# Kernel tuning notes

Measured on AMD Instinct MI355X. Metric: run time of the kernel, lower is better.

The kernel has to match this reference:

```python
import jax, jax.numpy as jnp
import numpy as np
from jax import lax

D_MODEL = 1024
D_STATE = 16
D_CONV = 4
EXPAND = 2
D_INNER = EXPAND * D_MODEL  # 2048
DT_RANK = -(-D_MODEL // 16)  # ceil = 64
BATCH = 2
T = 1024


def setup_inputs() -> dict:
    key = jax.random.key(0)
    ks = jax.random.split(key, 9)
    s = 0.02
    x = jax.random.normal(ks[0], (BATCH, T, D_MODEL), dtype=jnp.float32)
    W_in = jax.random.normal(ks[1], (D_MODEL, 2 * D_INNER), dtype=jnp.float32) * s
    conv_w = jax.random.normal(ks[2], (D_INNER, D_CONV), dtype=jnp.float32) * 0.2
    conv_b = jax.random.normal(ks[3], (D_INNER,), dtype=jnp.float32) * 0.02
    W_xproj = jax.random.normal(ks[4], (D_INNER, DT_RANK + 2 * D_STATE), dtype=jnp.float32) * s
    W_dt = jax.random.normal(ks[5], (DT_RANK, D_INNER), dtype=jnp.float32) * s
    b_dt = jax.random.normal(ks[6], (D_INNER,), dtype=jnp.float32) * 0.02
    A_log = jnp.broadcast_to(jnp.log(jnp.arange(1, D_STATE + 1, dtype=jnp.float32)), (D_INNER, D_STATE)).copy()
    D_param = jnp.ones((D_INNER,), dtype=jnp.float32)
    W_out = jax.random.normal(ks[7], (D_INNER, D_MODEL), dtype=jnp.float32) * s
    return {"x": x, "W_in": W_in, "conv_w": conv_w, "conv_b": conv_b,
            "W_xproj": W_xproj, "W_dt": W_dt, "b_dt": b_dt,
            "A_log": A_log, "D_param": D_param, "W_out": W_out}


def _silu(u):
    return u * jax.nn.sigmoid(u)


def _forward(x, W_in, conv_w, conv_b, W_xproj, W_dt, b_dt, A_log, D_param, W_out):
    B, Tlen, _ = x.shape
    # in_proj and split into x-branch and gate z
    xz = x @ W_in                                   # (B,T,2*d_inner)
    x_b, z = jnp.split(xz, 2, axis=-1)              # each (B,T,d_inner)
    # causal depthwise conv1d: y[t] = sum_k w[:,k] * x[t-d_conv+1+k]
    xpad = jnp.pad(x_b, ((0, 0), (D_CONV - 1, 0), (0, 0)))
    xc = conv_b
    for k in range(D_CONV):
        xc = xc + xpad[:, k:k + Tlen, :] * conv_w[:, k]
    xc = _silu(xc)                                  # (B,T,d_inner)
    # SSM parameter projections
    proj = xc @ W_xproj                             # (B,T,dt_rank+2*d_state)
    delta_raw = proj[..., :DT_RANK]
    B_in = proj[..., DT_RANK:DT_RANK + D_STATE]     # (B,T,d_state)
    C_in = proj[..., DT_RANK + D_STATE:]            # (B,T,d_state)
    delta = jax.nn.softplus(delta_raw @ W_dt + b_dt)  # (B,T,d_inner)
    A = -jnp.exp(A_log)                             # (d_inner,d_state)
    A_bar = jnp.exp(delta[..., None] * A)           # (B,T,d_inner,d_state)
    Bx = delta[..., None] * B_in[:, :, None, :] * xc[..., None]  # (B,T,d_inner,d_state)

    def step(h, ins):
        a_t, bx_t, c_t, xc_t = ins
        h = a_t * h + bx_t                          # (B,d_inner,d_state)
        y_t = jnp.einsum('bds,bs->bd', h, c_t) + D_param * xc_t
        return h, y_t

    h0 = jnp.zeros((B, D_INNER, D_STATE), dtype=x.dtype)
    ins = (jnp.swapaxes(A_bar, 0, 1), jnp.swapaxes(Bx, 0, 1),
           jnp.swapaxes(C_in, 0, 1), jnp.swapaxes(xc, 0, 1))
    _, ys = lax.scan(step, h0, ins)                 # ys: (T,B,d_inner)
    y = jnp.swapaxes(ys, 0, 1) * _silu(z)           # gated
    return y @ W_out                                # (B,T,d_model)


def reference(x, W_in, conv_w, conv_b, W_xproj, W_dt, b_dt, A_log, D_param, W_out):
    return _forward(x, W_in, conv_w, conv_b, W_xproj, W_dt, b_dt, A_log, D_param, W_out)
```

## Files before the change

kernel.cpp:

```cpp
#include <hip/hip_runtime.h>
#include <math.h>

#define BATCH   2
#define TLEN    1024
#define DMODEL  1024
#define DINNER  2048
#define DSTATE  16
#define DTRANK  64
#define NPROJ   (DTRANK + 2*DSTATE)
#define CH      16
#define NCH     (TLEN / CH)

typedef __attribute__((ext_vector_type(8))) short short8;
typedef __attribute__((ext_vector_type(4))) float f32x4;

__device__ __forceinline__ float siluf(float u) {
    return u / (1.0f + __expf(-u));
}
__device__ __forceinline__ float softplusf(float x) {
    return (x > 20.0f) ? x : log1pf(__expf(x));
}
__device__ __forceinline__ unsigned short f2bf(float f) {
    union { float f; unsigned u; } v; v.f = f;
    unsigned r = v.u + 0x7FFF + ((v.u >> 16) & 1);
    return (unsigned short)(r >> 16);
}
__device__ __forceinline__ float bf2f(unsigned short u) {
    union { unsigned u; float f; } v; v.u = (unsigned)u << 16;
    return v.f;
}

#define GLOAD_LDS16(g, l) \
  __builtin_amdgcn_global_load_lds( \
     (const __attribute__((address_space(1))) unsigned int*)(g), \
     (__attribute__((address_space(3))) unsigned int*)(l), 16, 0, 0)

template<int NFRAG, int OUTBF, int EPI>
__global__ __launch_bounds__(256)
void gemm_bf16(const unsigned short* __restrict__ A, int lda,
               const unsigned short* __restrict__ BT, int ldb,
               void* __restrict__ Cv, int ldc, int kchunk,
               const float* __restrict__ bias, size_t zstride)
{
    constexpr int BN = NFRAG * 32;
    __shared__ unsigned short As[128 * 32];
    __shared__ unsigned short Bs[BN * 32];

    const int nwg = gridDim.x * gridDim.y;
    int id = blockIdx.y * gridDim.x + blockIdx.x;
    {
        const int q = nwg >> 3, r = nwg & 7, xcd = id & 7, lid = id >> 3;
        id = (xcd < r ? xcd * (q + 1) : r * (q + 1) + (xcd - r) * q) + lid;
    }
    const int bx = id % gridDim.x, by = id / gridDim.x;

    const int tid  = threadIdx.x;
    const int wid  = tid >> 6;
    const int lane = tid & 63;
    const int brow = by * 128;
    const int bcol = bx * BN;
    const int kbeg = blockIdx.z * kchunk;
    const int wr = (wid >> 1) * 64;
    const int wc = (wid & 1) * (NFRAG * 16);
    const int lrow = lane & 15;
    const int lk   = (lane >> 4) * 8;

    f32x4 acc[4][NFRAG] = {};

    for (int k0 = kbeg; k0 < kbeg + kchunk; k0 += 32) {
        #pragma unroll
        for (int it = 0; it < 2; ++it) {
            const int c = it * 256 + tid;
            const unsigned short* g = A + (size_t)(brow + (c >> 2)) * lda + k0 + (c & 3) * 8;
            GLOAD_LDS16(g, As + (size_t)(it * 256 + wid * 64) * 8);
        }
        constexpr int BCH = BN * 4;
        #pragma unroll
        for (int it = 0; it < (BCH + 255) / 256; ++it) {
            const int c = it * 256 + tid;
            if (BCH % 256 == 0 || c < BCH) {
                const unsigned short* g = BT + (size_t)(bcol + (c >> 2)) * ldb + k0 + (c & 3) * 8;
                GLOAD_LDS16(g, Bs + (size_t)(it * 256 + wid * 64) * 8);
            }
        }
        __syncthreads();

        short8 af[4], bfr[NFRAG];
        #pragma unroll
        for (int m = 0; m < 4; ++m)
            af[m] = *(const short8*)(As + (size_t)(wr + m * 16 + lrow) * 32 + lk);
        #pragma unroll
        for (int n = 0; n < NFRAG; ++n)
            bfr[n] = *(const short8*)(Bs + (size_t)(wc + n * 16 + lrow) * 32 + lk);

        #pragma unroll
        for (int m = 0; m < 4; ++m)
            #pragma unroll
            for (int n = 0; n < NFRAG; ++n)
                acc[m][n] = __builtin_amdgcn_mfma_f32_16x16x32_bf16(af[m], bfr[n], acc[m][n], 0, 0, 0);
        __syncthreads();
    }

    const size_t zoff = (size_t)blockIdx.z * zstride;
    const int crow = (lane >> 4) * 4;
    #pragma unroll
    for (int m = 0; m < 4; ++m)
        #pragma unroll
        for (int n = 0; n < NFRAG; ++n) {
            const int gc = bcol + wc + n * 16 + lrow;
            const size_t coff = zoff + (size_t)(brow + wr + m * 16 + crow) * ldc + gc;
            #pragma unroll
            for (int r = 0; r < 4; ++r) {
                float v = acc[m][n][r];
                if (EPI == 1) v = softplusf(v + bias[gc]);
                if (OUTBF)
                    ((unsigned short*)Cv)[coff + (size_t)r * ldc] = f2bf(v);
                else
                    ((float*)Cv)[coff + (size_t)r * ldc] = v;
            }
        }
}

__global__ __launch_bounds__(256)
void reduce8_dual(const float* __restrict__ in, float* __restrict__ out,
                  unsigned short* __restrict__ draw, int n, size_t zstride)
{
    const int i = blockIdx.x * 256 + threadIdx.x;
    if (i >= n) return;
    float s = 0.f;
    #pragma unroll
    for (int z = 0; z < 8; ++z) s += in[(size_t)z * zstride + i];
    out[i] = s;
    const int row = i / NPROJ;
    const int col = i - row * NPROJ;
    if (col < DTRANK) draw[(size_t)row * DTRANK + col] = f2bf(s);
}

__global__ __launch_bounds__(256)
void cast_rn(const float* __restrict__ in, unsigned short* __restrict__ out)
{
    const int i = blockIdx.x * 256 + threadIdx.x;
    float4 v = ((const float4*)in)[i];
    union { unsigned short u[4]; uint2 v2; } o;
    o.u[0] = f2bf(v.x); o.u[1] = f2bf(v.y); o.u[2] = f2bf(v.z); o.u[3] = f2bf(v.w);
    ((uint2*)out)[i] = o.v2;
}

__global__ __launch_bounds__(256)
void transpose_cast(const float* __restrict__ in, unsigned short* __restrict__ out,
                    int R, int C)
{
    __shared__ float tile[32][33];
    const int tx = threadIdx.x & 31, ty = threadIdx.x >> 5;
    const int c0 = blockIdx.x * 32, r0 = blockIdx.y * 32;
    #pragma unroll
    for (int j = 0; j < 32; j += 8)
        tile[ty + j][tx] = in[(size_t)(r0 + ty + j) * C + c0 + tx];
    __syncthreads();
    #pragma unroll
    for (int j = 0; j < 32; j += 8)
        out[(size_t)(c0 + ty + j) * R + r0 + tx] = f2bf(tile[tx][ty + j]);
}

__global__ __launch_bounds__(256)
void conv_silu(const unsigned short* __restrict__ xz, const float* __restrict__ conv_w,
               const float* __restrict__ conv_b, unsigned short* __restrict__ xc)
{
    const int idx = blockIdx.x * 256 + threadIdx.x;
    const int d = idx & (DINNER - 1);
    const int t = (idx >> 11) & (TLEN - 1);
    const int b = idx >> 21;

    const unsigned short* xb = xz + (size_t)b * TLEN * (2*DINNER) + d;
    float s = conv_b[d];
    const float4 w = *(const float4*)(conv_w + d * 4);
    const float wk[4] = {w.x, w.y, w.z, w.w};
    #pragma unroll
    for (int k = 0; k < 4; ++k) {
        const int tt = t + k - 3;
        if (tt >= 0) s = fmaf(bf2f(xb[(size_t)tt * (2*DINNER)]), wk[k], s);
    }
    xc[idx] = f2bf(siluf(s));
}

__global__ __launch_bounds__(256)
void scan1(const unsigned short* __restrict__ delta, const unsigned short* __restrict__ xc,
           const float* __restrict__ proj, const float* __restrict__ A_log,
           float* __restrict__ hloc, float* __restrict__ sumdel)
{
    const int idx = blockIdx.x * 256 + threadIdx.x;
    const int d = idx & (DINNER - 1);
    const int c = (idx >> 11) & (NCH - 1);
    const int b = idx >> 17;

    float Aa[DSTATE];
    #pragma unroll
    for (int s = 0; s < DSTATE; ++s) Aa[s] = -__expf(A_log[d * DSTATE + s]);

    float h[DSTATE];
    #pragma unroll
    for (int s = 0; s < DSTATE; ++s) h[s] = 0.f;
    float sd = 0.f;

    const int t0 = c * CH;
    const unsigned short* dptr = delta + ((size_t)(b * TLEN + t0)) * DINNER + d;
    const unsigned short* xptr = xc    + ((size_t)(b * TLEN + t0)) * DINNER + d;
    const float* pptr = proj  + ((size_t)(b * TLEN + t0)) * NPROJ;

    for (int t = 0; t < CH; ++t) {
        const float dl = bf2f(dptr[(size_t)t * DINNER]);
        const float xv = bf2f(xptr[(size_t)t * DINNER]);
        const float dx = dl * xv;
        sd += dl;
        #pragma unroll
        for (int s = 0; s < DSTATE; ++s) {
            const float ab = __expf(dl * Aa[s]);
            const float Bv = pptr[t * NPROJ + DTRANK + s];
            h[s] = fmaf(ab, h[s], dx * Bv);
        }
    }
    const size_t base = (((size_t)(b * DINNER + d)) * NCH + c) * DSTATE;
    float4* hp = (float4*)(hloc + base);
    hp[0] = make_float4(h[0],  h[1],  h[2],  h[3]);
    hp[1] = make_float4(h[4],  h[5],  h[6],  h[7]);
    hp[2] = make_float4(h[8],  h[9],  h[10], h[11]);
    hp[3] = make_float4(h[12], h[13], h[14], h[15]);
    sumdel[(size_t)(b * DINNER + d) * NCH + c] = sd;
}

__global__ __launch_bounds__(256)
void scan_combine(const float* __restrict__ hloc, const float* __restrict__ sumdel,
                  const float* __restrict__ A_log, float* __restrict__ hstart)
{
    __shared__ float hl[64 * 17];
    __shared__ float hs[64 * 17];
    const int bd   = blockIdx.x;
    const int d    = bd & (DINNER - 1);
    const int tid  = threadIdx.x;
    const int lane = tid & 63;
    const int w    = tid >> 6;

    const size_t gbase = (size_t)bd * NCH * DSTATE;
    {
        const float4 v = ((const float4*)(hloc + gbase))[tid];
        const int c = tid >> 2, s0 = (tid & 3) * 4;
        hl[c*17 + s0+0] = v.x; hl[c*17 + s0+1] = v.y;
        hl[c*17 + s0+2] = v.z; hl[c*17 + s0+3] = v.w;
    }
    const float sd = sumdel[(size_t)bd * NCH + lane];
    __syncthreads();

    #pragma unroll
    for (int q = 0; q < 4; ++q) {
        const int s = w * 4 + q;
        const float Aa = -__expf(A_log[d * DSTATE + s]);
        float A  = __expf(Aa * sd);
        float Bv = hl[lane*17 + s];
        #pragma unroll
        for (int off = 1; off < 64; off <<= 1) {
            float Ap = __shfl_up(A, off);
            float Bp = __shfl_up(Bv, off);
            if (lane >= off) { Bv = fmaf(A, Bp, Bv); A *= Ap; }
        }
        float hsv = __shfl_up(Bv, 1);
        if (lane == 0) hsv = 0.f;
        hs[lane*17 + s] = hsv;
    }
    __syncthreads();
    {
        const int c = tid >> 2, s0 = (tid & 3) * 4;
        float4 v = make_float4(hs[c*17 + s0+0], hs[c*17 + s0+1],
                               hs[c*17 + s0+2], hs[c*17 + s0+3]);
        ((float4*)(hstart + gbase))[tid] = v;
    }
}

__global__ __launch_bounds__(256)
void scan2(const unsigned short* __restrict__ delta, const unsigned short* __restrict__ xc,
           const float* __restrict__ proj, const float* __restrict__ A_log,
           const float* __restrict__ D_param, const unsigned short* __restrict__ xz,
           const float* __restrict__ hstart, unsigned short* __restrict__ y)
{
    const int idx = blockIdx.x * 256 + threadIdx.x;
    const int d = idx & (DINNER - 1);
    const int c = (idx >> 11) & (NCH - 1);
    const int b = idx >> 17;

    float Aa[DSTATE];
    #pragma unroll
    for (int s = 0; s < DSTATE; ++s) Aa[s] = -__expf(A_log[d * DSTATE + s]);

    float h[DSTATE];
    const size_t hbase = (((size_t)(b * DINNER + d)) * NCH + c) * DSTATE;
    {
        const float4* hp = (const float4*)(hstart + hbase);
        float4 v0 = hp[0], v1 = hp[1], v2 = hp[2], v3 = hp[3];
        h[0]=v0.x; h[1]=v0.y; h[2]=v0.z; h[3]=v0.w;
        h[4]=v1.x; h[5]=v1.y; h[6]=v1.z; h[7]=v1.w;
        h[8]=v2.x; h[9]=v2.y; h[10]=v2.z; h[11]=v2.w;
        h[12]=v3.x; h[13]=v3.y; h[14]=v3.z; h[15]=v3.w;
    }

    const float Dp = D_param[d];
    const int t0 = c * CH;
    const unsigned short* dptr = delta + ((size_t)(b * TLEN + t0)) * DINNER + d;
    const unsigned short* xptr = xc    + ((size_t)(b * TLEN + t0)) * DINNER + d;
    const float* pptr = proj  + ((size_t)(b * TLEN + t0)) * NPROJ;
    const unsigned short* zptr = xz + ((size_t)(b * TLEN + t0)) * (2*DINNER) + DINNER + d;
    unsigned short* yptr = y + ((size_t)(b * TLEN + t0)) * DINNER + d;

    for (int t = 0; t < CH; ++t) {
        const float dl = bf2f(dptr[(size_t)t * DINNER]);
        const float xv = bf2f(xptr[(size_t)t * DINNER]);
        const float dx = dl * xv;
        float yt = 0.f;
        #pragma unroll
        for (int s = 0; s < DSTATE; ++s) {
            const float ab = __expf(dl * Aa[s]);
            const float Bv = pptr[t * NPROJ + DTRANK + s];
            h[s] = fmaf(ab, h[s], dx * Bv);
            const float Cv = pptr[t * NPROJ + DTRANK + DSTATE + s];
            yt = fmaf(h[s], Cv, yt);
        }
        yt = fmaf(Dp, xv, yt);
        const float z = bf2f(zptr[(size_t)t * (2*DINNER)]);
        yptr[(size_t)t * DINNER] = f2bf(yt * siluf(z));
    }
}

extern "C" void kernel_launch(void* const* d_in, const int* in_sizes, int n_in,
                              void* d_out, int out_size, void* d_ws, size_t ws_size,
                              hipStream_t stream)
{
    const float* x      = (const float*)d_in[0];
    const float* W_in   = (const float*)d_in[1];
    const float* conv_w = (const float*)d_in[2];
    const float* conv_b = (const float*)d_in[3];
    const float* W_xproj= (const float*)d_in[4];
    const float* W_dt   = (const float*)d_in[5];
    const float* b_dt   = (const float*)d_in[6];
    const float* A_log  = (const float*)d_in[7];
    const float* D_param= (const float*)d_in[8];
    const float* W_out  = (const float*)d_in[9];
    float* out = (float*)d_out;

    float* ws = (float*)d_ws;
    unsigned short* xz_bf    = (unsigned short*)ws;
    unsigned short* xc_bf    = (unsigned short*)(ws + 4194304);
    float*          proj     = ws + 6291456;
    unsigned short* delta_bf = (unsigned short*)(ws + 6488064);
    float*          hloc     = ws + 8585216;
    float*          sumdel   = ws + 12779520;
    float*          hstart   = ws + 13041664;
    float*          projp    = hloc;
    unsigned short* draw_bf  = (unsigned short*)(hloc + 1572864);
    unsigned short* yb_bf    = (unsigned short*)hloc;
    unsigned short* wt_out   = (unsigned short*)(hloc + 2097152);
    unsigned short* x_bf     = (unsigned short*)hstart;
    unsigned short* wt_in    = (unsigned short*)(hstart + 1048576);
    unsigned short* wxp_t    = (unsigned short*)(hstart + 3145728);
    unsigned short* wdt_t    = (unsigned short*)(hstart + 3244032);

    dim3 blk(256);

    cast_rn<<<2048, blk, 0, stream>>>(x, x_bf);
    transpose_cast<<<dim3(2*DINNER/32, DMODEL/32), blk, 0, stream>>>(W_in, wt_in, DMODEL, 2*DINNER);
    gemm_bf16<4,1,0><<<dim3(2*DINNER/128, 2048/128), blk, 0, stream>>>(
        x_bf, DMODEL, wt_in, DMODEL, xz_bf, 2*DINNER, DMODEL, nullptr, 0);

    conv_silu<<<(BATCH*TLEN*DINNER)/256, blk, 0, stream>>>(xz_bf, conv_w, conv_b, xc_bf);

    transpose_cast<<<dim3(NPROJ/32, DINNER/32), blk, 0, stream>>>(W_xproj, wxp_t, DINNER, NPROJ);
    gemm_bf16<3,0,0><<<dim3(1, 2048/128, 8), blk, 0, stream>>>(
        xc_bf, DINNER, wxp_t, DINNER, projp, NPROJ, DINNER/8, nullptr, 196608);
    reduce8_dual<<<768, blk, 0, stream>>>(projp, proj, draw_bf, 196608, 196608);

    transpose_cast<<<dim3(DINNER/32, DTRANK/32), blk, 0, stream>>>(W_dt, wdt_t, DTRANK, DINNER);
    gemm_bf16<4,1,1><<<dim3(2048/128, 2048/128), blk, 0, stream>>>(
        draw_bf, DTRANK, wdt_t, DTRANK, delta_bf, DINNER, DTRANK, b_dt, 0);

    scan1<<<(BATCH*NCH*DINNER)/256, blk, 0, stream>>>(delta_bf, xc_bf, proj, A_log, hloc, sumdel);
    scan_combine<<<BATCH*DINNER, blk, 0, stream>>>(hloc, sumdel, A_log, hstart);
    transpose_cast<<<dim3(DMODEL/32, DINNER/32), blk, 0, stream>>>(W_out, wt_out, DINNER, DMODEL);
    scan2<<<(BATCH*NCH*DINNER)/256, blk, 0, stream>>>(delta_bf, xc_bf, proj, A_log, D_param, xz_bf, hstart, yb_bf);

    gemm_bf16<2,0,0><<<dim3(DMODEL/64, 2048/128), blk, 0, stream>>>(
        yb_bf, DINNER, wt_out, DINNER, out, DMODEL, DINNER, nullptr, 0);
}
```

Baseline: 284.6 us.

## Fuse weight prep kernels, double scan chunk size, store chunk states in bf16

Merges the input cast and four weight transpose-casts into one prep kernel, which cuts several launches. Doubles the scan chunk length so there are half as many chunks, which halves the inter-chunk state traffic and shrinks the combine scan to 32 lanes. Stores per-chunk local and start states as bf16 instead of fp32, cutting their memory traffic at some precision cost. The workspace is re-laid out so buffers no longer alias, and scan1/scan2 now launch half as many threads, each doing more sequential work.

```diff
diff --git a/kernel.cpp b/kernel.cpp
--- a/kernel.cpp
+++ b/kernel.cpp
@@ -8,7 +8,7 @@
 #define DSTATE  16
 #define DTRANK  64
 #define NPROJ   (DTRANK + 2*DSTATE)
-#define CH      16
+#define CH      32
 #define NCH     (TLEN / CH)
 
 typedef __attribute__((ext_vector_type(8))) short short8;
@@ -121,6 +121,52 @@
         }
 }
 
+__device__ __forceinline__ void tile_transpose(float (*tile)[33],
+        const float* __restrict__ in, unsigned short* __restrict__ out,
+        int R, int C, int bx, int by, int tx, int ty)
+{
+    const int c0 = bx * 32, r0 = by * 32;
+    #pragma unroll
+    for (int j = 0; j < 32; j += 8)
+        tile[ty + j][tx] = in[(size_t)(r0 + ty + j) * C + c0 + tx];
+    __syncthreads();
+    #pragma unroll
+    for (int j = 0; j < 32; j += 8)
+        out[(size_t)(c0 + ty + j) * R + r0 + tx] = f2bf(tile[tx][ty + j]);
+}
+
+__global__ __launch_bounds__(256)
+void prep(const float* __restrict__ x, const float* __restrict__ W_in,
+          const float* __restrict__ W_xproj, const float* __restrict__ W_dt,
+          const float* __restrict__ W_out,
+          unsigned short* __restrict__ x_bf, unsigned short* __restrict__ wt_in,
+          unsigned short* __restrict__ wxp_t, unsigned short* __restrict__ wdt_t,
+          unsigned short* __restrict__ wt_out)
+{
+    __shared__ float tile[32][33];
+    const int blk = blockIdx.x;
+    const int tx = threadIdx.x & 31, ty = threadIdx.x >> 5;
+    if (blk < 2048) {
+        const int i = blk * 256 + threadIdx.x;
+        float4 v = ((const float4*)x)[i];
+        union { unsigned short u[4]; uint2 v2; } o;
+        o.u[0] = f2bf(v.x); o.u[1] = f2bf(v.y); o.u[2] = f2bf(v.z); o.u[3] = f2bf(v.w);
+        ((uint2*)x_bf)[i] = o.v2;
+    } else if (blk < 6144) {
+        const int lb = blk - 2048;
+        tile_transpose(tile, W_in, wt_in, DMODEL, 2*DINNER, lb % 128, lb / 128, tx, ty);
+    } else if (blk < 6336) {
+        const int lb = blk - 6144;
+        tile_transpose(tile, W_xproj, wxp_t, DINNER, NPROJ, lb % 3, lb / 3, tx, ty);
+    } else if (blk < 6464) {
+        const int lb = blk - 6336;
+        tile_transpose(tile, W_dt, wdt_t, DTRANK, DINNER, lb % 64, lb / 64, tx, ty);
+    } else {
+        const int lb = blk - 6464;
+        tile_transpose(tile, W_out, wt_out, DINNER, DMODEL, lb % 32, lb / 32, tx, ty);
+    }
+}
+
 __global__ __launch_bounds__(256)
 void reduce8_dual(const float* __restrict__ in, float* __restrict__ out,
                   unsigned short* __restrict__ draw, int n, size_t zstride)
@@ -137,32 +183,6 @@
 }
 
 __global__ __launch_bounds__(256)
-void cast_rn(const float* __restrict__ in, unsigned short* __restrict__ out)
-{
-    const int i = blockIdx.x * 256 + threadIdx.x;
-    float4 v = ((const float4*)in)[i];
-    union { unsigned short u[4]; uint2 v2; } o;
-    o.u[0] = f2bf(v.x); o.u[1] = f2bf(v.y); o.u[2] = f2bf(v.z); o.u[3] = f2bf(v.w);
-    ((uint2*)out)[i] = o.v2;
-}
-
-__global__ __launch_bounds__(256)
-void transpose_cast(const float* __restrict__ in, unsigned short* __restrict__ out,
-                    int R, int C)
-{
-    __shared__ float tile[32][33];
-    const int tx = threadIdx.x & 31, ty = threadIdx.x >> 5;
-    const int c0 = blockIdx.x * 32, r0 = blockIdx.y * 32;
-    #pragma unroll
-    for (int j = 0; j < 32; j += 8)
-        tile[ty + j][tx] = in[(size_t)(r0 + ty + j) * C + c0 + tx];
-    __syncthreads();
-    #pragma unroll
-    for (int j = 0; j < 32; j += 8)
-        out[(size_t)(c0 + ty + j) * R + r0 + tx] = f2bf(tile[tx][ty + j]);
-}
-
-__global__ __launch_bounds__(256)
 void conv_silu(const unsigned short* __restrict__ xz, const float* __restrict__ conv_w,
                const float* __restrict__ conv_b, unsigned short* __restrict__ xc)
 {
@@ -186,12 +206,12 @@
 __global__ __launch_bounds__(256)
 void scan1(const unsigned short* __restrict__ delta, const unsigned short* __restrict__ xc,
            const float* __restrict__ proj, const float* __restrict__ A_log,
-           float* __restrict__ hloc, float* __restrict__ sumdel)
+           unsigned short* __restrict__ hloc, float* __restrict__ sumdel)
 {
     const int idx = blockIdx.x * 256 + threadIdx.x;
     const int d = idx & (DINNER - 1);
     const int c = (idx >> 11) & (NCH - 1);
-    const int b = idx >> 17;
+    const int b = idx >> 16;
 
     float Aa[DSTATE];
     #pragma unroll
@@ -219,59 +239,57 @@
             h[s] = fmaf(ab, h[s], dx * Bv);
         }
     }
-    const size_t base = (((size_t)(b * DINNER + d)) * NCH + c) * DSTATE;
-    float4* hp = (float4*)(hloc + base);
-    hp[0] = make_float4(h[0],  h[1],  h[2],  h[3]);
-    hp[1] = make_float4(h[4],  h[5],  h[6],  h[7]);
-    hp[2] = make_float4(h[8],  h[9],  h[10], h[11]);
-    hp[3] = make_float4(h[12], h[13], h[14], h[15]);
+    unsigned u[8];
+    #pragma unroll
+    for (int i = 0; i < 8; ++i)
+        u[i] = (unsigned)f2bf(h[2*i]) | ((unsigned)f2bf(h[2*i+1]) << 16);
+    unsigned* hp = (unsigned*)hloc + (((size_t)(b * DINNER + d)) * NCH + c) * 8;
+    ((uint4*)hp)[0] = make_uint4(u[0], u[1], u[2], u[3]);
+    ((uint4*)hp)[1] = make_uint4(u[4], u[5], u[6], u[7]);
     sumdel[(size_t)(b * DINNER + d) * NCH + c] = sd;
 }
 
 __global__ __launch_bounds__(256)
-void scan_combine(const float* __restrict__ hloc, const float* __restrict__ sumdel,
-                  const float* __restrict__ A_log, float* __restrict__ hstart)
-{
-    __shared__ float hl[64 * 17];
-    __shared__ float hs[64 * 17];
-    const int bd   = blockIdx.x;
-    const int d    = bd & (DINNER - 1);
-    const int tid  = threadIdx.x;
-    const int lane = tid & 63;
-    const int w    = tid >> 6;
-
-    const size_t gbase = (size_t)bd * NCH * DSTATE;
+void scan_combine(const unsigned short* __restrict__ hloc, const float* __restrict__ sumdel,
+                  const float* __restrict__ A_log, unsigned short* __restrict__ hstart)
+{
+    __shared__ float hl[32 * 17];
+    __shared__ unsigned short hso[32 * 16];
+    const int bd  = blockIdx.x;
+    const int d   = bd & (DINNER - 1);
+    const int tid = threadIdx.x;
+
     {
-        const float4 v = ((const float4*)(hloc + gbase))[tid];
-        const int c = tid >> 2, s0 = (tid & 3) * 4;
-        hl[c*17 + s0+0] = v.x; hl[c*17 + s0+1] = v.y;
-        hl[c*17 + s0+2] = v.z; hl[c*17 + s0+3] = v.w;
-    }
-    const float sd = sumdel[(size_t)bd * NCH + lane];
+        const unsigned v = ((const unsigned*)hloc)[(size_t)bd * 256 + tid];
+        const int c = tid >> 3, s0 = (tid & 7) * 2;
+        hl[c*17 + s0]     = bf2f((unsigned short)(v & 0xFFFF));
+        hl[c*17 + s0 + 1] = bf2f((unsigned short)(v >> 16));
+    }
+    const int lane32 = tid & 31;
+    const int grp    = tid >> 5;
+    const float sdv = sumdel[(size_t)bd * NCH + lane32];
     __syncthreads();
 
     #pragma unroll
-    for (int q = 0; q < 4; ++q) {
-        const int s = w * 4 + q;
+    for (int q = 0; q < 2; ++q) {
+        const int s = grp * 2 + q;
         const float Aa = -__expf(A_log[d * DSTATE + s]);
-        float A  = __expf(Aa * sd);
-        float Bv = hl[lane*17 + s];
-        #pragma unroll
-        for (int off = 1; off < 64; off <<= 1) {
-            float Ap = __shfl_up(A, off);
-            float Bp = __shfl_up(Bv, off);
-            if (lane >= off) { Bv = fmaf(A, Bp, Bv); A *= Ap; }
-        }
-        float hsv = __shfl_up(Bv, 1);
-        if (lane == 0) hsv = 0.f;
-        hs[lane*17 + s] = hsv;
+        float A  = __expf(Aa * sdv);
+        float Bv = hl[lane32*17 + s];
+        #pragma unroll
+        for (int off = 1; off < 32; off <<= 1) {
+            float Ap = __shfl_up(A, off, 32);
+            float Bp = __shfl_up(Bv, off, 32);
+            if (lane32 >= off) { Bv = fmaf(A, Bp, Bv); A *= Ap; }
+        }
+        float hsv = __shfl_up(Bv, 1, 32);
+        if (lane32 == 0) hsv = 0.f;
+        hso[lane32*16 + s] = f2bf(hsv);
     }
     __syncthreads();
     {
-        const int c = tid >> 2, s0 = (tid & 3) * 4;
-        float4 v = make_float4(hs[c*17 + s0+0], hs[c*17 + s0+1],
-                               hs[c*17 + s0+2], hs[c*17 + s0+3]);
-        ((float4*)(hstart + gbase))[tid] = v;
+        const unsigned v = (unsigned)hso[tid*2] | ((unsigned)hso[tid*2+1] << 16);
+        ((unsigned*)hstart)[(size_t)bd * 256 + tid] = v;
     }
 }
 
@@ -279,26 +297,27 @@
 void scan2(const unsigned short* __restrict__ delta, const unsigned short* __restrict__ xc,
            const float* __restrict__ proj, const float* __restrict__ A_log,
            const float* __restrict__ D_param, const unsigned short* __restrict__ xz,
-           const float* __restrict__ hstart, unsigned short* __restrict__ y)
+           const unsigned short* __restrict__ hstart, unsigned short* __restrict__ y)
 {
     const int idx = blockIdx.x * 256 + threadIdx.x;
     const int d = idx & (DINNER - 1);
     const int c = (idx >> 11) & (NCH - 1);
-    const int b = idx >> 17;
+    const int b = idx >> 16;
 
     float Aa[DSTATE];
     #pragma unroll
     for (int s = 0; s < DSTATE; ++s) Aa[s] = -__expf(A_log[d * DSTATE + s]);
 
     float h[DSTATE];
-    const size_t hbase = (((size_t)(b * DINNER + d)) * NCH + c) * DSTATE;
     {
-        const float4* hp = (const float4*)(hstart + hbase);
-        float4 v0 = hp[0], v1 = hp[1], v2 = hp[2], v3 = hp[3];
-        h[0]=v0.x; h[1]=v0.y; h[2]=v0.z; h[3]=v0.w;
-        h[4]=v1.x; h[5]=v1.y; h[6]=v1.z; h[7]=v1.w;
-        h[8]=v2.x; h[9]=v2.y; h[10]=v2.z; h[11]=v2.w;
-        h[12]=v3.x; h[13]=v3.y; h[14]=v3.z; h[15]=v3.w;
+        const unsigned* hp = (const unsigned*)hstart + (((size_t)(b * DINNER + d)) * NCH + c) * 8;
+        uint4 v0 = ((const uint4*)hp)[0], v1 = ((const uint4*)hp)[1];
+        unsigned uu[8] = {v0.x, v0.y, v0.z, v0.w, v1.x, v1.y, v1.z, v1.w};
+        #pragma unroll
+        for (int i = 0; i < 8; ++i) {
+            h[2*i]   = bf2f((unsigned short)(uu[i] & 0xFFFF));
+            h[2*i+1] = bf2f((unsigned short)(uu[i] >> 16));
+        }
     }
 
     const float Dp = D_param[d];
@@ -345,43 +364,41 @@
     float* out = (float*)d_out;
 
     float* ws = (float*)d_ws;
-    unsigned short* xz_bf    = (unsigned short*)ws;
+    unsigned short* xz_bf    = (unsigned short*)(ws + 0);
     unsigned short* xc_bf    = (unsigned short*)(ws + 4194304);
     float*          proj     = ws + 6291456;
     unsigned short* delta_bf = (unsigned short*)(ws + 6488064);
-    float*          hloc     = ws + 8585216;
-    float*          sumdel   = ws + 12779520;
-    float*          hstart   = ws + 13041664;
-    float*          projp    = hloc;
-    unsigned short* draw_bf  = (unsigned short*)(hloc + 1572864);
-    unsigned short* yb_bf    = (unsigned short*)hloc;
-    unsigned short* wt_out   = (unsigned short*)(hloc + 2097152);
-    unsigned short* x_bf     = (unsigned short*)hstart;
-    unsigned short* wt_in    = (unsigned short*)(hstart + 1048576);
-    unsigned short* wxp_t    = (unsigned short*)(hstart + 3145728);
-    unsigned short* wdt_t    = (unsigned short*)(hstart + 3244032);
+    unsigned short* hloc     = (unsigned short*)(ws + 8585216);
+    float*          sumdel   = ws + 9633792;
+    unsigned short* hstart   = (unsigned short*)(ws + 9764864);
+    unsigned short* x_bf     = (unsigned short*)(ws + 10813440);
+    unsigned short* wt_in    = (unsigned short*)(ws + 11862016);
+    unsigned short* wxp_t    = (unsigned short*)(ws + 13959168);
+    unsigned short* wdt_t    = (unsigned short*)(ws + 14057472);
+    unsigned short* wt_out   = (unsigned short*)(ws + 14123008);
+    float*          projp    = ws + 15171584;
+    unsigned short* draw_bf  = (unsigned short*)(ws + 16744448);
+    unsigned short* yb_bf    = (unsigned short*)(ws + 16809984);
 
     dim3 blk(256);
 
-    cast_rn<<<2048, blk, 0, stream>>>(x, x_bf);
-    transpose_cast<<<dim3(2*DINNER/32, DMODEL/32), blk, 0, stream>>>(W_in, wt_in, DMODEL, 2*DINNER);
+    prep<<<8512, blk, 0, stream>>>(x, W_in, W_xproj, W_dt, W_out,
+                                   x_bf, wt_in, wxp_t, wdt_t, wt_out);
+
     gemm_bf16<4,1,0><<<dim3(2*DINNER/128, 2048/128), blk, 0, stream>>>(
         x_bf, DMODEL, wt_in, DMODEL, xz_bf, 2*DINNER, DMODEL, nullptr, 0);
 
     conv_silu<<<(BATCH*TLEN*DINNER)/256, blk, 0, stream>>>(xz_bf, conv_w, conv_b, xc_bf);
 
-    transpose_cast<<<dim3(NPROJ/32, DINNER/32), blk, 0, stream>>>(W_xproj, wxp_t, DINNER, NPROJ);
     gemm_bf16<3,0,0><<<dim3(1, 2048/128, 8), blk, 0, stream>>>(
         xc_bf, DINNER, wxp_t, DINNER, projp, NPROJ, DINNER/8, nullptr, 196608);
     reduce8_dual<<<768, blk, 0, stream>>>(projp, proj, draw_bf, 196608, 196608);
 
-    transpose_cast<<<dim3(DINNER/32, DTRANK/32), blk, 0, stream>>>(W_dt, wdt_t, DTRANK, DINNER);
     gemm_bf16<4,1,1><<<dim3(2048/128, 2048/128), blk, 0, stream>>>(
         draw_bf, DTRANK, wdt_t, DTRANK, delta_bf, DINNER, DTRANK, b_dt, 0);
 
     scan1<<<(BATCH*NCH*DINNER)/256, blk, 0, stream>>>(delta_bf, xc_bf, proj, A_log, hloc, sumdel);
     scan_combine<<<BATCH*DINNER, blk, 0, stream>>>(hloc, sumdel, A_log, hstart);
-    transpose_cast<<<dim3(DMODEL/32, DINNER/32), blk, 0, stream>>>(W_out, wt_out, DINNER, DMODEL);
     scan2<<<(BATCH*NCH*DINNER)/256, blk, 0, stream>>>(delta_bf, xc_bf, proj, A_log, D_param, xz_bf, hstart, yb_bf);
 
     gemm_bf16<2,0,0><<<dim3(DMODEL/64, 2048/128), blk, 0, stream>>>(
```

Result: faster. 274.3 us (-3.6%).
